# Kernel optimization log

Hardware: AMD Instinct MI355X
Metric: run time of the kernel (lower is better)

Reference implementation:

```python
import jax, jax.numpy as jnp
import numpy as np


def setup_inputs() -> dict:
    key = jax.random.key(0)
    k1, k2, k3 = jax.random.split(key, 3)
    B, C2, H, W = 8, 128, 28, 28   # resnet18 layer2 output for 224x224 input
    C3, H3, W3 = 256, 14, 14       # resnet18 layer3 output
    M = 30000                      # memory bank patches (post-coreset)
    f2 = jax.random.normal(k1, (B, C2, H, W), dtype=jnp.float32)
    f3 = jax.random.normal(k2, (B, C3, H3, W3), dtype=jnp.float32)
    memory_bank = jax.random.normal(k3, (M, C2 + C3), dtype=jnp.float32)
    return {"f2": f2, "f3": f3, "memory_bank": memory_bank}


def reference(f2, f3, memory_bank):
    """PatchCore predict: multi-layer embed + brute-force 1-NN euclidean distance.

    f2: [B,C2,H,W] (layer2 feats), f3: [B,C3,H3,W3] (layer3 feats),
    memory_bank: [M, C2+C3]. Returns (patch_scores [B,H,W], img_scores [B]).
    """
    B, C2, H, W = f2.shape
    C3 = f3.shape[1]
    # F.interpolate(..., mode='bilinear', align_corners=False) == jax.image.resize bilinear
    f3_up = jax.image.resize(f3, (B, C3, H, W), method="bilinear")
    emb = jnp.concatenate([f2, f3_up], axis=1)            # [B,C,H,W], C=C2+C3
    C = C2 + C3
    patches = emb.transpose(0, 2, 3, 1).reshape(-1, C)    # [N,C], N=B*H*W
    x_sq = jnp.sum(patches * patches, axis=-1, keepdims=True)      # [N,1]
    m_sq = jnp.sum(memory_bank * memory_bank, axis=-1)[None, :]    # [1,M]
    d2 = x_sq + m_sq - 2.0 * (patches @ memory_bank.T)             # [N,M]
    dists = jnp.sqrt(jnp.maximum(d2, 1e-12))
    nn_dist = jnp.min(dists, axis=1)                               # 1-NN (n_neighbors=1)
    patch_scores = nn_dist.reshape(B, H, W)
    img_scores = jnp.max(patch_scores.reshape(B, -1), axis=1)
    return patch_scores, img_scores
```

## Files before the change

kernel.cpp:

```cpp
#include <hip/hip_runtime.h>
#include <hip/hip_bf16.h>
#include <stdint.h>

typedef float f32x4 __attribute__((ext_vector_type(4)));
typedef short bf16x8 __attribute__((ext_vector_type(8)));

#define NPATCH 6272
#define CTOT   384
#define MBANK  30000
#define MROWS  6400
#define NCOLS  30720
#define NCT    120
#define W      12
#define NCG    10

#define PF2B   16
#define PF3B   32
#define PBANKB (NCOLS / 4)
#define NPREP  (PF2B + PF3B + PBANKB)

__global__ __launch_bounds__(256) void prep_kernel(
    const float* __restrict__ f2, const float* __restrict__ f3,
    const float* __restrict__ mb,
    __hip_bfloat16* __restrict__ A, __hip_bfloat16* __restrict__ Bb,
    float* __restrict__ m_sq)
{
  __shared__ float tile[64 * 197];
  const int t = threadIdx.x;
  const int lane = t & 63;
  const int grp  = t >> 6;

  if (blockIdx.x < PF2B) {
    const int b  = blockIdx.x >> 1;
    const int c0 = (blockIdx.x & 1) * 64;
    const float* src = f2 + ((size_t)b * 128 + c0) * 784;
    __hip_bfloat16* dst = A + (size_t)b * 784 * CTOT + c0;
    for (int hw0 = 0; hw0 < 784; hw0 += 64) {
      const int nhw = (784 - hw0 < 64) ? (784 - hw0) : 64;
      __syncthreads();
      #pragma unroll
      for (int k = 0; k < 16; ++k) {
        const int c = grp * 16 + k;
        if (lane < nhw) tile[c * 65 + lane] = src[(size_t)c * 784 + hw0 + lane];
      }
      __syncthreads();
      #pragma unroll
      for (int k = 0; k < 16; ++k) {
        const int r = grp * 16 + k;
        if (r < nhw) dst[(size_t)(hw0 + r) * CTOT + lane] = __float2bfloat16(tile[lane * 65 + r]);
      }
    }
  } else if (blockIdx.x < PF2B + PF3B) {
    const int blk = blockIdx.x - PF2B;
    const int b  = blk >> 2;
    const int c0 = (blk & 3) * 64;
    const float* src = f3 + ((size_t)b * 256 + c0) * 196;
    for (int idx = t; idx < 64 * 196; idx += 256) {
      const int c = idx / 196, p = idx - c * 196;
      tile[c * 197 + p] = src[(size_t)c * 196 + p];
    }
    __syncthreads();
    __hip_bfloat16* dst = A + (size_t)b * 784 * CTOT + 128 + c0;
    for (int hw0 = 0; hw0 < 784; hw0 += 64) {
      #pragma unroll
      for (int k = 0; k < 16; ++k) {
        const int r = grp * 16 + k;
        const int hw = hw0 + r;
        if (hw < 784) {
          const int h = hw / 28, w = hw - h * 28;
          int h0, h1, w0i, w1i; float wh0, wh1, ww0, ww1;
          if (h & 1) { int q = h >> 1; h0 = q; h1 = (q + 1 < 14) ? q + 1 : 13; wh0 = 0.75f; wh1 = 0.25f; }
          else       { int q = h >> 1; h0 = (q > 0) ? q - 1 : 0; h1 = q;       wh0 = 0.25f; wh1 = 0.75f; }
          if (w & 1) { int q = w >> 1; w0i = q; w1i = (q + 1 < 14) ? q + 1 : 13; ww0 = 0.75f; ww1 = 0.25f; }
          else       { int q = w >> 1; w0i = (q > 0) ? q - 1 : 0; w1i = q;       ww0 = 0.25f; ww1 = 0.75f; }
          const float* tl = &tile[lane * 197];
          const float v = wh0 * (ww0 * tl[h0 * 14 + w0i] + ww1 * tl[h0 * 14 + w1i]) +
                          wh1 * (ww0 * tl[h1 * 14 + w0i] + ww1 * tl[h1 * 14 + w1i]);
          dst[(size_t)hw * CTOT + lane] = __float2bfloat16(v);
        }
      }
    }
  } else {
    const int m = (blockIdx.x - PF2B - PF3B) * 4 + grp;
    if (m < MBANK) {
      float ssum = 0.f;
      #pragma unroll
      for (int j = 0; j < 3; ++j) {
        const int c = j * 128 + lane * 2;
        const float2 v = *(const float2*)&mb[(size_t)m * CTOT + c];
        short2 o;
        o.x = (short)__bfloat16_as_ushort(__float2bfloat16(v.x));
        o.y = (short)__bfloat16_as_ushort(__float2bfloat16(v.y));
        *(short2*)&Bb[(size_t)m * CTOT + c] = o;
        ssum += v.x * v.x + v.y * v.y;
      }
      #pragma unroll
      for (int off = 32; off; off >>= 1) ssum += __shfl_xor(ssum, off);
      if (lane == 0) m_sq[m] = ssum;
    } else {
      #pragma unroll
      for (int j = 0; j < 6; ++j) Bb[(size_t)m * CTOT + j * 64 + lane] = __float2bfloat16(0.f);
      if (lane == 0) m_sq[m] = __uint_as_float(0x7f800000u);
    }
  }
}

__device__ __forceinline__ void gl_lds16(const void* g, void* l) {
  __builtin_amdgcn_global_load_lds(
      (const __attribute__((address_space(1))) uint32_t*)g,
      (__attribute__((address_space(3))) uint32_t*)l, 16, 0, 0);
}

__global__ __launch_bounds__(512, 2) void gemm_min_kernel(
    const __hip_bfloat16* __restrict__ A, const __hip_bfloat16* __restrict__ B,
    const float* __restrict__ m_sq, float* __restrict__ partial)
{
  __shared__ __align__(16) short As[2][256 * 64];
  __shared__ __align__(16) short Bs[2][256 * 64];
  __shared__ float redm[4][256];
  const int tid  = threadIdx.x;
  const int lane = tid & 63;
  const int wid  = tid >> 6;
  const int wr = wid >> 2;
  const int wc = wid & 3;
  const int row0 = blockIdx.y * 256;
  const int ct0  = blockIdx.x * W;

  f32x4 acc[8][4];
  #pragma unroll
  for (int i = 0; i < 8; ++i)
    #pragma unroll
    for (int j = 0; j < 4; ++j) acc[i][j] = (f32x4){0.f, 0.f, 0.f, 0.f};

  auto stage_pair = [&](int c2, int kt2, int buf, int j) {
    const int k0 = kt2 * 64;
    const int cb = j * 512 + wid * 64;
    const int cc = cb + lane;
    const int r  = cc >> 3;
    const int ch = (cc & 7) ^ (r & 7);
    gl_lds16(A + (size_t)(row0 + r) * CTOT + k0 + ch * 8, &As[buf][cb * 8]);
    gl_lds16(B + ((size_t)(ct0 + c2) * 256 + r) * CTOT + k0 + ch * 8, &Bs[buf][cb * 8]);
  };

  #pragma unroll
  for (int j = 0; j < 4; ++j) stage_pair(0, 0, 0, j);
  #pragma unroll
  for (int j = 0; j < 4; ++j) stage_pair(0, 1, 1, j);
  asm volatile("s_waitcnt vmcnt(8)" ::: "memory");
  __builtin_amdgcn_s_barrier();

  const int sw = lane & 7;
  const int rA = wr * 128 + (lane & 15);
  const int rB = wc * 64 + (lane & 15);
  const int kq = lane >> 4;
  const int ch0 = (kq ^ sw) << 4;
  const int ch1 = ((4 + kq) ^ sw) << 4;

  float msq[4];
  float runmin = __uint_as_float(0x7f800000u);

  for (int c = 0; c < W; ++c) {
    #pragma unroll
    for (int kt = 0; kt < 6; ++kt) {
      const int cur = kt & 1;
      const char* lA = (const char*)As[cur];
      const char* lB = (const char*)Bs[cur];
      const int kt2 = (kt == 5) ? 0 : kt + 1;
      const int c2  = (kt == 5) ? c + 1 : c;
      const bool st = !(c == 0 && kt == 0) && !(c == W - 1 && kt == 5);
      bf16x8 a0[8], b0[4], a1[8], b1[4];

      #pragma unroll
      for (int ni = 0; ni < 4; ++ni) b0[ni] = *(const bf16x8*)(lB + (rB + ni * 16) * 128 + ch0);
      #pragma unroll
      for (int mi = 0; mi < 4; ++mi) a0[mi] = *(const bf16x8*)(lA + (rA + mi * 16) * 128 + ch0);
      if (kt == 0) {
        const int colb = (ct0 + c) * 256 + wc * 64 + (lane & 15);
        #pragma unroll
        for (int ni = 0; ni < 4; ++ni) msq[ni] = m_sq[colb + ni * 16];
      }
      if (st) stage_pair(c2, kt2, cur ^ 1, 0);
      __builtin_amdgcn_s_barrier();
      asm volatile("s_waitcnt lgkmcnt(0)" ::: "memory");
      __builtin_amdgcn_s_setprio(1);
      #pragma unroll
      for (int mi = 0; mi < 4; ++mi)
        #pragma unroll
        for (int ni = 0; ni < 4; ++ni)
          acc[mi][ni] = __builtin_amdgcn_mfma_f32_16x16x32_bf16(a0[mi], b0[ni], acc[mi][ni], 0, 0, 0);
      __builtin_amdgcn_s_setprio(0);
      __builtin_amdgcn_s_barrier();

      #pragma unroll
      for (int mi = 4; mi < 8; ++mi) a0[mi] = *(const bf16x8*)(lA + (rA + mi * 16) * 128 + ch0);
      if (st) stage_pair(c2, kt2, cur ^ 1, 1);
      __builtin_amdgcn_s_barrier();
      asm volatile("s_waitcnt lgkmcnt(0)" ::: "memory");
      __builtin_amdgcn_s_setprio(1);
      #pragma unroll
      for (int mi = 4; mi < 8; ++mi)
        #pragma unroll
        for (int ni = 0; ni < 4; ++ni)
          acc[mi][ni] = __builtin_amdgcn_mfma_f32_16x16x32_bf16(a0[mi], b0[ni], acc[mi][ni], 0, 0, 0);
      __builtin_amdgcn_s_setprio(0);
      __builtin_amdgcn_s_barrier();

      #pragma unroll
      for (int ni = 0; ni < 4; ++ni) b1[ni] = *(const bf16x8*)(lB + (rB + ni * 16) * 128 + ch1);
      #pragma unroll
      for (int mi = 0; mi < 4; ++mi) a1[mi] = *(const bf16x8*)(lA + (rA + mi * 16) * 128 + ch1);
      if (st) stage_pair(c2, kt2, cur ^ 1, 2);
      __builtin_amdgcn_s_barrier();
      asm volatile("s_waitcnt lgkmcnt(0)" ::: "memory");
      __builtin_amdgcn_s_setprio(1);
      #pragma unroll
      for (int mi = 0; mi < 4; ++mi)
        #pragma unroll
        for (int ni = 0; ni < 4; ++ni)
          acc[mi][ni] = __builtin_amdgcn_mfma_f32_16x16x32_bf16(a1[mi], b1[ni], acc[mi][ni], 0, 0, 0);
      __builtin_amdgcn_s_setprio(0);
      __builtin_amdgcn_s_barrier();

      #pragma unroll
      for (int mi = 4; mi < 8; ++mi) a1[mi] = *(const bf16x8*)(lA + (rA + mi * 16) * 128 + ch1);
      if (st) stage_pair(c2, kt2, cur ^ 1, 3);
      __builtin_amdgcn_s_barrier();
      asm volatile("s_waitcnt lgkmcnt(0)" ::: "memory");
      __builtin_amdgcn_s_setprio(1);
      #pragma unroll
      for (int mi = 4; mi < 8; ++mi)
        #pragma unroll
        for (int ni = 0; ni < 4; ++ni)
          acc[mi][ni] = __builtin_amdgcn_mfma_f32_16x16x32_bf16(a1[mi], b1[ni], acc[mi][ni], 0, 0, 0);
      __builtin_amdgcn_s_setprio(0);

      if (kt == 5) {
        #pragma unroll
        for (int mi = 0; mi < 8; ++mi) {
          #pragma unroll
          for (int r = 0; r < 4; ++r) {
            float tv = msq[0] - 2.f * acc[mi][0][r];
            #pragma unroll
            for (int ni = 1; ni < 4; ++ni) tv = fminf(tv, msq[ni] - 2.f * acc[mi][ni][r]);
            tv = fminf(tv, __shfl_xor(tv, 1));
            tv = fminf(tv, __shfl_xor(tv, 2));
            tv = fminf(tv, __shfl_xor(tv, 4));
            tv = fminf(tv, __shfl_xor(tv, 8));
            if ((lane & 15) == 0)
              redm[wc][wr * 128 + mi * 16 + ((lane >> 4) << 2) + r] = tv;
          }
          #pragma unroll
          for (int ni = 0; ni < 4; ++ni) acc[mi][ni] = (f32x4){0.f, 0.f, 0.f, 0.f};
        }
        __syncthreads();
        if (lane < 32) {
          const int rl = wid * 32 + lane;
          const float m01 = fminf(redm[0][rl], redm[1][rl]);
          const float m23 = fminf(redm[2][rl], redm[3][rl]);
          runmin = fminf(runmin, fminf(m01, m23));
        }
        if (c == W - 1 && lane < 32)
          partial[(size_t)blockIdx.x * MROWS + row0 + wid * 32 + lane] = runmin;
      } else {
        asm volatile("s_waitcnt vmcnt(0)" ::: "memory");
        __builtin_amdgcn_s_barrier();
      }
    }
  }
}

__global__ __launch_bounds__(256) void finalize_kernel(
    const float* __restrict__ partial, const __hip_bfloat16* __restrict__ A,
    float* __restrict__ out)
{
  const int b = blockIdx.x;
  const int t = threadIdx.x;
  __shared__ float red[4];
  float lmax = 0.f;
  if (t < 196) {
    const int n0 = b * 784 + t * 4;
    float4 mn = {__uint_as_float(0x7f800000u), __uint_as_float(0x7f800000u),
                 __uint_as_float(0x7f800000u), __uint_as_float(0x7f800000u)};
    for (int g = 0; g < NCG; ++g) {
      const float4 p = *(const float4*)&partial[(size_t)g * MROWS + n0];
      mn.x = fminf(mn.x, p.x); mn.y = fminf(mn.y, p.y);
      mn.z = fminf(mn.z, p.z); mn.w = fminf(mn.w, p.w);
    }
    float xs[4];
    #pragma unroll
    for (int r = 0; r < 4; ++r) {
      const bf16x8* ap = (const bf16x8*)(A + (size_t)(n0 + r) * CTOT);
      float s = 0.f;
      for (int j = 0; j < 48; ++j) {
        const bf16x8 v = ap[j];
        #pragma unroll
        for (int e = 0; e < 8; ++e) {
          const float f = __uint_as_float(((unsigned)(unsigned short)v[e]) << 16);
          s += f * f;
        }
      }
      xs[r] = s;
    }
    float4 o;
    o.x = sqrtf(fmaxf(mn.x + xs[0], 1e-12f));
    o.y = sqrtf(fmaxf(mn.y + xs[1], 1e-12f));
    o.z = sqrtf(fmaxf(mn.z + xs[2], 1e-12f));
    o.w = sqrtf(fmaxf(mn.w + xs[3], 1e-12f));
    *(float4*)&out[n0] = o;
    lmax = fmaxf(fmaxf(o.x, o.y), fmaxf(o.z, o.w));
  }
  #pragma unroll
  for (int off = 32; off; off >>= 1) lmax = fmaxf(lmax, __shfl_xor(lmax, off));
  if ((t & 63) == 0) red[t >> 6] = lmax;
  __syncthreads();
  if (t == 0)
    out[6272 + b] = fmaxf(fmaxf(red[0], red[1]), fmaxf(red[2], red[3]));
}

extern "C" void kernel_launch(void* const* d_in, const int* in_sizes, int n_in,
                              void* d_out, int out_size, void* d_ws, size_t ws_size,
                              hipStream_t stream)
{
  const float* f2 = (const float*)d_in[0];
  const float* f3 = (const float*)d_in[1];
  const float* mb = (const float*)d_in[2];
  float* out = (float*)d_out;

  uint8_t* ws = (uint8_t*)d_ws;
  __hip_bfloat16* A  = (__hip_bfloat16*)(ws);
  __hip_bfloat16* Bb = (__hip_bfloat16*)(ws + 4915200);
  float* m_sq   = (float*)(ws + 28508160);
  float* partial = (float*)(ws + 28631040);

  hipLaunchKernelGGL(prep_kernel, dim3(NPREP), dim3(256), 0, stream,
                     f2, f3, mb, A, Bb, m_sq);
  hipLaunchKernelGGL(gemm_min_kernel, dim3(NCG, MROWS / 256), dim3(512), 0, stream,
                     A, Bb, m_sq, partial);
  hipLaunchKernelGGL(finalize_kernel, dim3(8), dim3(256), 0, stream,
                     partial, A, out);
}
```

Before: 441.8 us.

## Rebalance GEMM grid to 8x25 column groups and precompute patch norms in prep

Changes the column split from 10 groups of 12 tiles to 8 groups of 15, giving a 200-block 1D grid. This better fits the CU count (256) and leaves no second partial wave. All four staging loads for the next k-tile are now issued at the first sub-step instead of being spread across the four MFMA phases. Patch squared norms are computed during prep with wave shuffles and stored as six partial sums, so finalize no longer rereads the bf16 A matrix. The trade-off is less overlap of global loads with MFMA work and extra shuffle reductions in prep.

Result: slower. 504.3 us (+14.1%).

```diff
diff --git a/kernel.cpp b/kernel.cpp
--- a/kernel.cpp
+++ b/kernel.cpp
@@ -10,9 +10,8 @@
 #define MBANK  30000
 #define MROWS  6400
 #define NCOLS  30720
-#define NCT    120
-#define W      12
-#define NCG    10
+#define NCG    8
+#define W      15
 
 #define PF2B   16
 #define PF3B   32
@@ -23,7 +22,7 @@
     const float* __restrict__ f2, const float* __restrict__ f3,
     const float* __restrict__ mb,
     __hip_bfloat16* __restrict__ A, __hip_bfloat16* __restrict__ Bb,
-    float* __restrict__ m_sq)
+    float* __restrict__ m_sq, float* __restrict__ x_sq_part)
 {
   __shared__ float tile[64 * 197];
   const int t = threadIdx.x;
@@ -32,9 +31,11 @@
 
   if (blockIdx.x < PF2B) {
     const int b  = blockIdx.x >> 1;
-    const int c0 = (blockIdx.x & 1) * 64;
+    const int seg = blockIdx.x & 1;
+    const int c0 = seg * 64;
     const float* src = f2 + ((size_t)b * 128 + c0) * 784;
     __hip_bfloat16* dst = A + (size_t)b * 784 * CTOT + c0;
+    float* xsp = x_sq_part + (size_t)seg * MROWS + b * 784;
     for (int hw0 = 0; hw0 < 784; hw0 += 64) {
       const int nhw = (784 - hw0 < 64) ? (784 - hw0) : 64;
       __syncthreads();
@@ -47,13 +48,21 @@
       #pragma unroll
       for (int k = 0; k < 16; ++k) {
         const int r = grp * 16 + k;
-        if (r < nhw) dst[(size_t)(hw0 + r) * CTOT + lane] = __float2bfloat16(tile[lane * 65 + r]);
+        if (r < nhw) {
+          const float v = tile[lane * 65 + r];
+          dst[(size_t)(hw0 + r) * CTOT + lane] = __float2bfloat16(v);
+          float s = v * v;
+          #pragma unroll
+          for (int off = 32; off; off >>= 1) s += __shfl_xor(s, off);
+          if (lane == 0) xsp[hw0 + r] = s;
+        }
       }
     }
   } else if (blockIdx.x < PF2B + PF3B) {
     const int blk = blockIdx.x - PF2B;
     const int b  = blk >> 2;
-    const int c0 = (blk & 3) * 64;
+    const int cseg = blk & 3;
+    const int c0 = cseg * 64;
     const float* src = f3 + ((size_t)b * 256 + c0) * 196;
     for (int idx = t; idx < 64 * 196; idx += 256) {
       const int c = idx / 196, p = idx - c * 196;
@@ -61,6 +70,7 @@
     }
     __syncthreads();
     __hip_bfloat16* dst = A + (size_t)b * 784 * CTOT + 128 + c0;
+    float* xsp = x_sq_part + (size_t)(2 + cseg) * MROWS + b * 784;
     for (int hw0 = 0; hw0 < 784; hw0 += 64) {
       #pragma unroll
       for (int k = 0; k < 16; ++k) {
@@ -77,6 +87,10 @@
           const float v = wh0 * (ww0 * tl[h0 * 14 + w0i] + ww1 * tl[h0 * 14 + w1i]) +
                           wh1 * (ww0 * tl[h1 * 14 + w0i] + ww1 * tl[h1 * 14 + w1i]);
           dst[(size_t)hw * CTOT + lane] = __float2bfloat16(v);
+          float s = v * v;
+          #pragma unroll
+          for (int off = 32; off; off >>= 1) s += __shfl_xor(s, off);
+          if (lane == 0) xsp[hw] = s;
         }
       }
     }
@@ -123,8 +137,10 @@
   const int wid  = tid >> 6;
   const int wr = wid >> 2;
   const int wc = wid & 3;
-  const int row0 = blockIdx.y * 256;
-  const int ct0  = blockIdx.x * W;
+  const int gx = blockIdx.x & 7;
+  const int gy = blockIdx.x >> 3;
+  const int row0 = gy * 256;
+  const int ct0  = gx * W;
 
   f32x4 acc[8][4];
   #pragma unroll
@@ -132,20 +148,21 @@
     #pragma unroll
     for (int j = 0; j < 4; ++j) acc[i][j] = (f32x4){0.f, 0.f, 0.f, 0.f};
 
-  auto stage_pair = [&](int c2, int kt2, int buf, int j) {
+  auto stage_tile = [&](int c2, int kt2, int buf) {
     const int k0 = kt2 * 64;
-    const int cb = j * 512 + wid * 64;
-    const int cc = cb + lane;
-    const int r  = cc >> 3;
-    const int ch = (cc & 7) ^ (r & 7);
-    gl_lds16(A + (size_t)(row0 + r) * CTOT + k0 + ch * 8, &As[buf][cb * 8]);
-    gl_lds16(B + ((size_t)(ct0 + c2) * 256 + r) * CTOT + k0 + ch * 8, &Bs[buf][cb * 8]);
+    #pragma unroll
+    for (int j = 0; j < 4; ++j) {
+      const int cb = j * 512 + wid * 64;
+      const int cc = cb + lane;
+      const int r  = cc >> 3;
+      const int ch = (cc & 7) ^ (r & 7);
+      gl_lds16(A + (size_t)(row0 + r) * CTOT + k0 + ch * 8, &As[buf][cb * 8]);
+      gl_lds16(B + ((size_t)(ct0 + c2) * 256 + r) * CTOT + k0 + ch * 8, &Bs[buf][cb * 8]);
+    }
   };
 
-  #pragma unroll
-  for (int j = 0; j < 4; ++j) stage_pair(0, 0, 0, j);
-  #pragma unroll
-  for (int j = 0; j < 4; ++j) stage_pair(0, 1, 1, j);
+  stage_tile(0, 0, 0);
+  stage_tile(0, 1, 1);
   asm volatile("s_waitcnt vmcnt(8)" ::: "memory");
   __builtin_amdgcn_s_barrier();
 
@@ -179,7 +196,7 @@
         #pragma unroll
         for (int ni = 0; ni < 4; ++ni) msq[ni] = m_sq[colb + ni * 16];
       }
-      if (st) stage_pair(c2, kt2, cur ^ 1, 0);
+      if (st) stage_tile(c2, kt2, cur ^ 1);
       __builtin_amdgcn_s_barrier();
       asm volatile("s_waitcnt lgkmcnt(0)" ::: "memory");
       __builtin_amdgcn_s_setprio(1);
@@ -193,7 +210,6 @@
 
       #pragma unroll
       for (int mi = 4; mi < 8; ++mi) a0[mi] = *(const bf16x8*)(lA + (rA + mi * 16) * 128 + ch0);
-      if (st) stage_pair(c2, kt2, cur ^ 1, 1);
       __builtin_amdgcn_s_barrier();
       asm volatile("s_waitcnt lgkmcnt(0)" ::: "memory");
       __builtin_amdgcn_s_setprio(1);
@@ -209,7 +225,6 @@
       for (int ni = 0; ni < 4; ++ni) b1[ni] = *(const bf16x8*)(lB + (rB + ni * 16) * 128 + ch1);
       #pragma unroll
       for (int mi = 0; mi < 4; ++mi) a1[mi] = *(const bf16x8*)(lA + (rA + mi * 16) * 128 + ch1);
-      if (st) stage_pair(c2, kt2, cur ^ 1, 2);
       __builtin_amdgcn_s_barrier();
       asm volatile("s_waitcnt lgkmcnt(0)" ::: "memory");
       __builtin_amdgcn_s_setprio(1);
@@ -223,7 +238,6 @@
 
       #pragma unroll
       for (int mi = 4; mi < 8; ++mi) a1[mi] = *(const bf16x8*)(lA + (rA + mi * 16) * 128 + ch1);
-      if (st) stage_pair(c2, kt2, cur ^ 1, 3);
       __builtin_amdgcn_s_barrier();
       asm volatile("s_waitcnt lgkmcnt(0)" ::: "memory");
       __builtin_amdgcn_s_setprio(1);
@@ -260,7 +274,7 @@
           runmin = fminf(runmin, fminf(m01, m23));
         }
         if (c == W - 1 && lane < 32)
-          partial[(size_t)blockIdx.x * MROWS + row0 + wid * 32 + lane] = runmin;
+          partial[(size_t)gx * MROWS + row0 + wid * 32 + lane] = runmin;
       } else {
         asm volatile("s_waitcnt vmcnt(0)" ::: "memory");
         __builtin_amdgcn_s_barrier();
@@ -270,7 +284,7 @@
 }
 
 __global__ __launch_bounds__(256) void finalize_kernel(
-    const float* __restrict__ partial, const __hip_bfloat16* __restrict__ A,
+    const float* __restrict__ partial, const float* __restrict__ x_sq_part,
     float* __restrict__ out)
 {
   const int b = blockIdx.x;
@@ -286,26 +300,17 @@
       mn.x = fminf(mn.x, p.x); mn.y = fminf(mn.y, p.y);
       mn.z = fminf(mn.z, p.z); mn.w = fminf(mn.w, p.w);
     }
-    float xs[4];
+    float4 xs = {0.f, 0.f, 0.f, 0.f};
     #pragma unroll
-    for (int r = 0; r < 4; ++r) {
-      const bf16x8* ap = (const bf16x8*)(A + (size_t)(n0 + r) * CTOT);
-      float s = 0.f;
-      for (int j = 0; j < 48; ++j) {
-        const bf16x8 v = ap[j];
-        #pragma unroll
-        for (int e = 0; e < 8; ++e) {
-          const float f = __uint_as_float(((unsigned)(unsigned short)v[e]) << 16);
-          s += f * f;
-        }
-      }
-      xs[r] = s;
+    for (int s = 0; s < 6; ++s) {
+      const float4 p = *(const float4*)&x_sq_part[(size_t)s * MROWS + n0];
+      xs.x += p.x; xs.y += p.y; xs.z += p.z; xs.w += p.w;
     }
     float4 o;
-    o.x = sqrtf(fmaxf(mn.x + xs[0], 1e-12f));
-    o.y = sqrtf(fmaxf(mn.y + xs[1], 1e-12f));
-    o.z = sqrtf(fmaxf(mn.z + xs[2], 1e-12f));
-    o.w = sqrtf(fmaxf(mn.w + xs[3], 1e-12f));
+    o.x = sqrtf(fmaxf(mn.x + xs.x, 1e-12f));
+    o.y = sqrtf(fmaxf(mn.y + xs.y, 1e-12f));
+    o.z = sqrtf(fmaxf(mn.z + xs.z, 1e-12f));
+    o.w = sqrtf(fmaxf(mn.w + xs.w, 1e-12f));
     *(float4*)&out[n0] = o;
     lmax = fmaxf(fmaxf(o.x, o.y), fmaxf(o.z, o.w));
   }
@@ -329,13 +334,14 @@
   uint8_t* ws = (uint8_t*)d_ws;
   __hip_bfloat16* A  = (__hip_bfloat16*)(ws);
   __hip_bfloat16* Bb = (__hip_bfloat16*)(ws + 4915200);
-  float* m_sq   = (float*)(ws + 28508160);
-  float* partial = (float*)(ws + 28631040);
+  float* m_sq     = (float*)(ws + 28508160);
+  float* partial  = (float*)(ws + 28631040);
+  float* x_sq_part = (float*)(ws + 28835840);
 
   hipLaunchKernelGGL(prep_kernel, dim3(NPREP), dim3(256), 0, stream,
-                     f2, f3, mb, A, Bb, m_sq);
-  hipLaunchKernelGGL(gemm_min_kernel, dim3(NCG, MROWS / 256), dim3(512), 0, stream,
+                     f2, f3, mb, A, Bb, m_sq, x_sq_part);
+  hipLaunchKernelGGL(gemm_min_kernel, dim3(NCG * 25), dim3(512), 0, stream,
                      A, Bb, m_sq, partial);
   hipLaunchKernelGGL(finalize_kernel, dim3(8), dim3(256), 0, stream,
-                     partial, A, out);
-}
+                     partial, x_sq_part, out);
+}
```
